# Optimization experiments

Hardware: AMD Instinct MI355X
Metric: run time of the kernel (lower is better)

## Reference

```python
import jax, jax.numpy as jnp
import numpy as np

HEADS = 16
DIM_HEAD = 64
SCALE = DIM_HEAD ** -0.5


def setup_inputs() -> dict:
    key = jax.random.key(0)
    ks = jax.random.split(key, 6)
    B, Nq, Nkv, D = 2, 512, 4096, 1024
    inner = HEADS * DIM_HEAD  # 1024
    s = 1.0 / np.sqrt(D)
    return {
        "q": jax.random.normal(ks[0], (B, Nq, D), jnp.float32),
        "kv": jax.random.normal(ks[1], (B, Nkv, D), jnp.float32),
        "mask": jnp.ones((B, Nkv), dtype=bool),
        "Wq": jax.random.normal(ks[2], (D, inner), jnp.float32) * s,
        "Wkv": jax.random.normal(ks[3], (D, 2 * inner), jnp.float32) * s,
        "Wo": jax.random.normal(ks[4], (inner, D), jnp.float32) * (1.0 / np.sqrt(inner)),
        "bo": jnp.zeros((D,), jnp.float32),
    }


def reference(q, kv, mask, Wq, Wkv, Wo, bo):
    B, Nq, D = q.shape
    Nkv = kv.shape[1]
    h, dh = HEADS, DIM_HEAD
    # projections
    qh = (q @ Wq).reshape(B, Nq, h, dh).transpose(0, 2, 1, 3)        # (B,h,Nq,dh)
    kvp = kv @ Wkv                                                    # (B,Nkv,2*inner)
    k, v = jnp.split(kvp, 2, axis=-1)
    kh = k.reshape(B, Nkv, h, dh).transpose(0, 2, 1, 3)              # (B,h,Nkv,dh)
    vh = v.reshape(B, Nkv, h, dh).transpose(0, 2, 1, 3)
    # scaled dot-product cross-attention
    attn = jnp.einsum("bhqd,bhkd->bhqk", qh, kh) * SCALE             # (B,h,Nq,Nkv)
    neg_inf = jnp.finfo(attn.dtype).min
    attn = jnp.where(mask[:, None, None, :], attn, neg_inf)
    attn = jax.nn.softmax(attn, axis=-1)
    out = jnp.einsum("bhqk,bhkd->bhqd", attn, vh)                    # (B,h,Nq,dh)
    out = out.transpose(0, 2, 1, 3).reshape(B, Nq, h * dh)
    return out @ Wo + bo
```

## Files before the change

### kernel.cpp

```cpp
#include <hip/hip_runtime.h>
#include <string.h>
#include <math.h>

typedef unsigned short u16;
typedef __bf16 bf16x8 __attribute__((ext_vector_type(8)));
typedef float floatx4 __attribute__((ext_vector_type(4)));

#define HEADS  16
#define DH     64
#define BATCH  2
#define NQ     512
#define NKV    4096
#define DMODEL 1024
#define INNER  1024
#define SCALE  0.125f
#define LOG2E  1.4426950408889634f
#define FM     12.0f
#define SPLIT  4
#define KEYS_PER_PART (NKV / SPLIT)
#define CH (KEYS_PER_PART / 64)

__device__ __forceinline__ u16 f2bf(float f) {
  union { __bf16 h; u16 u; } v; v.h = (__bf16)f; return v.u;
}

__device__ __forceinline__ void gll16(const u16* g, u16* l) {
  __builtin_amdgcn_global_load_lds(
      (const __attribute__((address_space(1))) unsigned int*)g,
      (__attribute__((address_space(3))) unsigned int*)l, 16, 0, 0);
}

__global__ __launch_bounds__(256) void prep(const float* __restrict__ q,
                                            const float* __restrict__ kv,
                                            const float* __restrict__ Wq,
                                            const float* __restrict__ Wkv,
                                            const float* __restrict__ Wo,
                                            u16* __restrict__ qb,
                                            u16* __restrict__ kvb,
                                            u16* __restrict__ Wqt,
                                            u16* __restrict__ Wkvt,
                                            u16* __restrict__ Wot) {
  __shared__ float tile[32][33];
  const int bx = blockIdx.x, tid = threadIdx.x;
  if (bx < 4608) {
    const float* x; u16* y; size_t i;
    if (bx < 512) { x = q;  y = qb;  i = (size_t)bx * 256 + tid; }
    else          { x = kv; y = kvb; i = (size_t)(bx - 512) * 256 + tid; }
    const float4* p = (const float4*)x + i * 2;
    float4 a = p[0], b = p[1];
    union { u16 s[8]; uint4 v; } o;
    o.s[0] = f2bf(a.x); o.s[1] = f2bf(a.y); o.s[2] = f2bf(a.z); o.s[3] = f2bf(a.w);
    o.s[4] = f2bf(b.x); o.s[5] = f2bf(b.y); o.s[6] = f2bf(b.z); o.s[7] = f2bf(b.w);
    *(uint4*)(y + i * 8) = o.v;
    return;
  }
  const float* W; u16* Wt; int K, N, n0, k0, t;
  if (bx < 5632)      { t = bx - 4608; W = Wq;  Wt = Wqt;  K = 1024; N = 1024; n0 = (t & 31) * 32; k0 = (t >> 5) * 32; }
  else if (bx < 7680) { t = bx - 5632; W = Wkv; Wt = Wkvt; K = 1024; N = 2048; n0 = (t & 63) * 32; k0 = (t >> 6) * 32; }
  else                { t = bx - 7680; W = Wo;  Wt = Wot;  K = 1024; N = 1024; n0 = (t & 31) * 32; k0 = (t >> 5) * 32; }
  const int tx = tid & 31, ty = tid >> 5;
  for (int i = 0; i < 32; i += 8)
    tile[ty + i][tx] = W[(size_t)(k0 + ty + i) * N + n0 + tx];
  __syncthreads();
  for (int i = 0; i < 32; i += 8)
    Wt[(size_t)(n0 + ty + i) * K + k0 + tx] = f2bf(tile[tx][ty + i]);
}

__global__ __launch_bounds__(256) void gemm_kv(const u16* __restrict__ A,
                                               const u16* __restrict__ Bt,
                                               u16* __restrict__ Kb,
                                               u16* __restrict__ vT) {
  const int K = DMODEL;
  __shared__ __align__(16) u16 As[128 * 64];
  __shared__ __align__(16) u16 Bs[128 * 64];
  const int tid  = threadIdx.x;
  const int lane = tid & 63, wave = tid >> 6;
  const int wr = wave >> 1, wc = wave & 1;
  const int l16 = lane & 15, quad = lane >> 4;
  const int bm = blockIdx.y, bn = blockIdx.x;
  const int r8 = lane >> 3;
  const int kb8 = (lane & 7) ^ r8;
  const u16* aP = A  + ((size_t)bm * 128 + wave * 8 + r8) * K + kb8 * 8;
  const u16* bP = Bt + ((size_t)bn * 128 + wave * 8 + r8) * K + kb8 * 8;

  floatx4 acc[4][4] = {};
  for (int k0 = 0; k0 < K; k0 += 64) {
#pragma unroll
    for (int p = 0; p < 4; ++p) {
      gll16(aP + (size_t)p * 32 * K + k0, As + p * 2048 + wave * 512);
      gll16(bP + (size_t)p * 32 * K + k0, Bs + p * 2048 + wave * 512);
    }
    __syncthreads();
    bf16x8 af[4][2], bfr[4][2];
#pragma unroll
    for (int i = 0; i < 4; ++i)
#pragma unroll
      for (int h2 = 0; h2 < 2; ++h2)
        af[i][h2] = *(const bf16x8*)&As[(wr * 64 + i * 16 + l16) * 64 +
                                        (((h2 * 4 + quad) ^ (l16 & 7)) << 3)];
#pragma unroll
    for (int j = 0; j < 4; ++j)
#pragma unroll
      for (int h2 = 0; h2 < 2; ++h2)
        bfr[j][h2] = *(const bf16x8*)&Bs[(wc * 64 + j * 16 + l16) * 64 +
                                         (((h2 * 4 + quad) ^ (l16 & 7)) << 3)];
#pragma unroll
    for (int i = 0; i < 4; ++i)
#pragma unroll
      for (int j = 0; j < 4; ++j) {
        acc[i][j] = __builtin_amdgcn_mfma_f32_16x16x32_bf16(af[i][0], bfr[j][0], acc[i][j], 0, 0, 0);
        acc[i][j] = __builtin_amdgcn_mfma_f32_16x16x32_bf16(af[i][1], bfr[j][1], acc[i][j], 0, 0, 0);
      }
    __syncthreads();
  }
  if (bn < 8) {
#pragma unroll
    for (int i = 0; i < 4; ++i) {
      const int rowb = bm * 128 + wr * 64 + i * 16 + quad * 4;
#pragma unroll
      for (int j = 0; j < 4; ++j) {
        const int col = bn * 128 + wc * 64 + j * 16 + l16;
#pragma unroll
        for (int r = 0; r < 4; ++r)
          Kb[(size_t)(rowb + r) * 1024 + col] = f2bf(acc[i][j][r]);
      }
    }
  } else {
    const int b = bm >> 5;
    const int tokb = (bm & 31) * 128;
#pragma unroll
    for (int i = 0; i < 4; ++i) {
      const int tok0 = tokb + wr * 64 + i * 16 + quad * 4;
#pragma unroll
      for (int j = 0; j < 4; ++j) {
        const int d = (bn - 8) * 128 + wc * 64 + j * 16 + l16;
        union { u16 s[4]; uint2 v; } pk;
#pragma unroll
        for (int r = 0; r < 4; ++r) pk.s[r] = f2bf(acc[i][j][r]);
        *(uint2*)(vT + ((size_t)(b * 1024 + d)) * NKV + tok0) = pk.v;
      }
    }
  }
}

template<bool OUT_BF16>
__global__ __launch_bounds__(256) void gemm64(const u16* __restrict__ A,
                                              const u16* __restrict__ Bt,
                                              float* __restrict__ Cf,
                                              u16* __restrict__ Cb,
                                              const float* __restrict__ bias,
                                              int M, int N, int K) {
  __shared__ __align__(16) u16 As[64 * 64];
  __shared__ __align__(16) u16 Bs[64 * 64];
  const int tid = threadIdx.x;
  const int lane = tid & 63, wave = tid >> 6;
  const int wr = wave >> 1, wc = wave & 1;
  const int l16 = lane & 15, quad = lane >> 4;
  const int bm = blockIdx.y, bn = blockIdx.x;
  const int r0 = tid >> 3;
  const int kbs = (tid & 7) ^ (r0 & 7);
  const u16* aP0 = A  + ((size_t)bm * 64 + r0)      * K + kbs * 8;
  const u16* aP1 = A  + ((size_t)bm * 64 + r0 + 32) * K + kbs * 8;
  const u16* bP0 = Bt + ((size_t)bn * 64 + r0)      * K + kbs * 8;
  const u16* bP1 = Bt + ((size_t)bn * 64 + r0 + 32) * K + kbs * 8;
  u16* ldsA0 = As + wave * 512;
  u16* ldsA1 = As + 2048 + wave * 512;
  u16* ldsB0 = Bs + wave * 512;
  u16* ldsB1 = Bs + 2048 + wave * 512;

  floatx4 acc[2][2] = {};
  for (int k0 = 0; k0 < K; k0 += 64) {
    gll16(aP0 + k0, ldsA0);
    gll16(aP1 + k0, ldsA1);
    gll16(bP0 + k0, ldsB0);
    gll16(bP1 + k0, ldsB1);
    __syncthreads();
    bf16x8 af[2][2], bfr[2][2];
#pragma unroll
    for (int i = 0; i < 2; ++i)
#pragma unroll
      for (int kk = 0; kk < 2; ++kk)
        af[i][kk] = *(const bf16x8*)&As[(wr * 32 + i * 16 + l16) * 64 +
                                        (((kk * 4 + quad) ^ (l16 & 7)) << 3)];
#pragma unroll
    for (int j = 0; j < 2; ++j)
#pragma unroll
      for (int kk = 0; kk < 2; ++kk)
        bfr[j][kk] = *(const bf16x8*)&Bs[(wc * 32 + j * 16 + l16) * 64 +
                                         (((kk * 4 + quad) ^ (l16 & 7)) << 3)];
#pragma unroll
    for (int i = 0; i < 2; ++i)
#pragma unroll
      for (int j = 0; j < 2; ++j) {
        acc[i][j] = __builtin_amdgcn_mfma_f32_16x16x32_bf16(af[i][0], bfr[j][0], acc[i][j], 0, 0, 0);
        acc[i][j] = __builtin_amdgcn_mfma_f32_16x16x32_bf16(af[i][1], bfr[j][1], acc[i][j], 0, 0, 0);
      }
    __syncthreads();
  }
#pragma unroll
  for (int i = 0; i < 2; ++i) {
    const int rowb = bm * 64 + wr * 32 + i * 16 + quad * 4;
#pragma unroll
    for (int j = 0; j < 2; ++j) {
      const int col = bn * 64 + wc * 32 + j * 16 + l16;
#pragma unroll
      for (int r = 0; r < 4; ++r) {
        const size_t idx = (size_t)(rowb + r) * N + col;
        if (OUT_BF16) Cb[idx] = f2bf(acc[i][j][r]);
        else          Cf[idx] = acc[i][j][r] + bias[col];
      }
    }
  }
}

__global__ __launch_bounds__(256) void attn_part(const u16* __restrict__ Qh,
                                                 const u16* __restrict__ Kb,
                                                 const u16* __restrict__ vT,
                                                 const int* __restrict__ mask,
                                                 float* __restrict__ Opart,
                                                 float* __restrict__ Mst,
                                                 float* __restrict__ Lst) {
  __shared__ __align__(16) u16 Ks[64 * 64];
  __shared__ __align__(16) u16 Vs[2][64 * 64];
  __shared__ __align__(16) u16 QP[4608];
  __shared__ float Msk[64];
  const int tid = threadIdx.x;
  const int lane = tid & 63, w = tid >> 6;
  const int l16 = lane & 15, quad = lane >> 4;
  const int part = blockIdx.x & (SPLIT - 1);
  const int qt = (blockIdx.x >> 2) & 7;
  const int h  = (blockIdx.x >> 5) & 15;
  const int b  = blockIdx.x >> 9;
  const int rs = tid >> 2, d0 = (tid & 3) * 16;
  u16* Ps = QP + w * 1152;

  const int r8 = lane >> 3;
  const int kb8 = (lane & 7) ^ (r8 & 7);
  const int key00 = part * KEYS_PER_PART;
  const u16* kSrc = Kb + ((size_t)(b * NKV + key00 + w * 8 + r8)) * 1024 + h * DH + kb8 * 8;
  const u16* vSrc = vT + ((size_t)((b * 16 + h) * 64 + w * 8 + r8)) * NKV + key00 + kb8 * 8;
  u16* ldsK0 = Ks + w * 512;
  u16* ldsK1 = Ks + 2048 + w * 512;
  const int koA = (quad ^ (l16 & 7)) << 3;
  const int koB = ((quad + 4) ^ (l16 & 7)) << 3;

  bf16x8 bones;
  {
    union { u16 s[8]; bf16x8 v; } t1;
    const u16 o1 = (l16 == 0) ? (u16)0x3F80 : (u16)0;
#pragma unroll
    for (int i = 0; i < 8; ++i) t1.s[i] = o1;
    bones = t1.v;
  }

  {
    const uint4* p = (const uint4*)(Qh + ((size_t)(b * NQ + qt * 64 + rs)) * INNER + h * DH + d0);
    *(uint4*)&QP[rs * 72 + d0]     = p[0];
    *(uint4*)&QP[rs * 72 + d0 + 8] = p[1];
  }
  gll16(kSrc, ldsK0);
  gll16(kSrc + 32768, ldsK1);
  gll16(vSrc, Vs[0] + w * 512);
  gll16(vSrc + (size_t)32 * NKV, Vs[0] + 2048 + w * 512);
  float mk0 = 0.f;
  if (tid < 64) mk0 = (mask[(size_t)b * NKV + key00 + tid] != 0) ? -FM : -1e30f;
  __syncthreads();
  bf16x8 aq0 = *(const bf16x8*)&QP[(w * 16 + l16) * 72 + quad * 8];
  bf16x8 aq1 = *(const bf16x8*)&QP[(w * 16 + l16) * 72 + 32 + quad * 8];
  if (tid < 64) Msk[tid] = mk0;
  __syncthreads();

  floatx4 o[4] = {};
  floatx4 lacc = {0.f, 0.f, 0.f, 0.f};
  const float SC = SCALE * LOG2E;

  for (int c = 0; c < CH; ++c) {
    const u16* Vcur = Vs[c & 1];
#pragma unroll
    for (int nt = 0; nt < 4; ++nt) {
      bf16x8 b0 = *(const bf16x8*)&Ks[(nt * 16 + l16) * 64 + koA];
      bf16x8 b1 = *(const bf16x8*)&Ks[(nt * 16 + l16) * 64 + koB];
      floatx4 t = {0.f, 0.f, 0.f, 0.f};
      t = __builtin_amdgcn_mfma_f32_16x16x32_bf16(aq0, b0, t, 0, 0, 0);
      t = __builtin_amdgcn_mfma_f32_16x16x32_bf16(aq1, b1, t, 0, 0, 0);
      const float mk = Msk[nt * 16 + l16];
#pragma unroll
      for (int r = 0; r < 4; ++r)
        Ps[(quad * 4 + r) * 72 + nt * 16 + l16] = f2bf(exp2f(t[r] * SC + mk));
    }
    __syncthreads();
    if (c + 1 < CH) {
      gll16(kSrc + (size_t)(c + 1) * 65536, ldsK0);
      gll16(kSrc + (size_t)(c + 1) * 65536 + 32768, ldsK1);
      u16* vdst = Vs[(c + 1) & 1];
      gll16(vSrc + (c + 1) * 64, vdst + w * 512);
      gll16(vSrc + (c + 1) * 64 + (size_t)32 * NKV, vdst + 2048 + w * 512);
      if (tid < 64)
        Msk[tid] = (mask[(size_t)b * NKV + key00 + (c + 1) * 64 + tid] != 0) ? -FM : -1e30f;
    }
    bf16x8 ap0 = *(const bf16x8*)&Ps[l16 * 72 + quad * 8];
    bf16x8 ap1 = *(const bf16x8*)&Ps[l16 * 72 + 32 + quad * 8];
    lacc = __builtin_amdgcn_mfma_f32_16x16x32_bf16(ap0, bones, lacc, 0, 0, 0);
    lacc = __builtin_amdgcn_mfma_f32_16x16x32_bf16(ap1, bones, lacc, 0, 0, 0);
#pragma unroll
    for (int dt = 0; dt < 4; ++dt) {
      bf16x8 bv0 = *(const bf16x8*)&Vcur[(dt * 16 + l16) * 64 + koA];
      bf16x8 bv1 = *(const bf16x8*)&Vcur[(dt * 16 + l16) * 64 + koB];
      o[dt] = __builtin_amdgcn_mfma_f32_16x16x32_bf16(ap0, bv0, o[dt], 0, 0, 0);
      o[dt] = __builtin_amdgcn_mfma_f32_16x16x32_bf16(ap1, bv1, o[dt], 0, 0, 0);
    }
    __syncthreads();
  }
  const int pid = blockIdx.x;
#pragma unroll
  for (int r = 0; r < 4; ++r) {
    const int q = w * 16 + quad * 4 + r;
    if (l16 == 0) { Mst[pid * 64 + q] = FM; Lst[pid * 64 + q] = lacc[r]; }
#pragma unroll
    for (int dt = 0; dt < 4; ++dt)
      Opart[(size_t)pid * 4096 + q * 64 + dt * 16 + l16] = o[dt][r];
  }
}

__global__ __launch_bounds__(256) void attn_combine(const float* __restrict__ Opart,
                                                    const float* __restrict__ Mst,
                                                    const float* __restrict__ Lst,
                                                    u16* __restrict__ Out) {
  const int x = blockIdx.x;
  const int t = threadIdx.x;
  const int q = t >> 2, db = (t & 3) * 16;
  const int b = x >> 7, h = (x >> 3) & 15, qt = x & 7;
  float ms[SPLIT], ls[SPLIT];
#pragma unroll
  for (int s = 0; s < SPLIT; ++s) {
    ms[s] = Mst[(size_t)(x * SPLIT + s) * 64 + q];
    ls[s] = Lst[(size_t)(x * SPLIT + s) * 64 + q];
  }
  float M = fmaxf(fmaxf(ms[0], ms[1]), fmaxf(ms[2], ms[3]));
  float wgt[SPLIT], L = 0.f;
#pragma unroll
  for (int s = 0; s < SPLIT; ++s) { wgt[s] = exp2f(ms[s] - M); L += wgt[s] * ls[s]; }
  const float inv = 1.0f / L;
  float acc[16] = {};
#pragma unroll
  for (int s = 0; s < SPLIT; ++s) {
    const float4* p = (const float4*)&Opart[(size_t)(x * SPLIT + s) * 4096 + q * 64 + db];
    const float ws = wgt[s];
#pragma unroll
    for (int i = 0; i < 4; ++i) {
      float4 v = p[i];
      acc[i * 4 + 0] += ws * v.x; acc[i * 4 + 1] += ws * v.y;
      acc[i * 4 + 2] += ws * v.z; acc[i * 4 + 3] += ws * v.w;
    }
  }
  union { u16 s[16]; uint4 v[2]; } ou;
#pragma unroll
  for (int i = 0; i < 16; ++i) ou.s[i] = f2bf(acc[i] * inv);
  u16* dst = Out + ((size_t)(b * NQ + qt * 64 + q)) * INNER + h * DH + db;
  *(uint4*)dst = ou.v[0]; *(uint4*)(dst + 8) = ou.v[1];
}

extern "C" void kernel_launch(void* const* d_in, const int* in_sizes, int n_in,
                              void* d_out, int out_size, void* d_ws, size_t ws_size,
                              hipStream_t stream) {
  const float* q    = (const float*)d_in[0];
  const float* kv   = (const float*)d_in[1];
  const int*   mask = (const int*)d_in[2];
  const float* Wq   = (const float*)d_in[3];
  const float* Wkv  = (const float*)d_in[4];
  const float* Wo   = (const float*)d_in[5];
  const float* bo   = (const float*)d_in[6];
  float* out = (float*)d_out;

  char* ws = (char*)d_ws;
  u16*   qb    = (u16*)(ws);
  u16*   kvb   = (u16*)(ws + (2u << 20));
  float* Mst   = (float*)(ws);
  float* Lst   = (float*)(ws + (256u << 10));
  float* Opart = (float*)(ws + (2u << 20));
  u16* Wqt  = (u16*)(ws + (18u << 20));
  u16* Wkvt = (u16*)(ws + (20u << 20));
  u16* Wot  = (u16*)(ws + (24u << 20));
  u16* qh   = (u16*)(ws + (26u << 20));
  u16* Kb   = (u16*)(ws + (28u << 20));
  u16* vT   = (u16*)(ws + (44u << 20));
  u16* attn = (u16*)(ws + (60u << 20));

  prep<<<dim3(8704), 256, 0, stream>>>(q, kv, Wq, Wkv, Wo, qb, kvb, Wqt, Wkvt, Wot);
  gemm64<true><<<dim3(INNER / 64, (BATCH * NQ) / 64), 256, 0, stream>>>(
      qb, Wqt, nullptr, qh, nullptr, BATCH * NQ, INNER, DMODEL);
  gemm_kv<<<dim3(16, 64), 256, 0, stream>>>(kvb, Wkvt, Kb, vT);
  attn_part<<<dim3(BATCH * HEADS * (NQ / 64) * SPLIT), 256, 0, stream>>>(
      qh, Kb, vT, mask, Opart, Mst, Lst);
  attn_combine<<<dim3(BATCH * HEADS * (NQ / 64)), 256, 0, stream>>>(Opart, Mst, Lst, attn);
  gemm64<false><<<dim3(DMODEL / 64, (BATCH * NQ) / 64), 256, 0, stream>>>(
      attn, Wot, out, nullptr, bo, BATCH * NQ, DMODEL, INNER);
}
```

Baseline: 214.0 us.

## Rewrite KV GEMM with 256x128 tiles, triple-buffered async loads, and XCD-aware block remap

```diff
diff --git a/kernel.cpp b/kernel.cpp
--- a/kernel.cpp
+++ b/kernel.cpp
@@ -66,81 +66,112 @@
     Wt[(size_t)(n0 + ty + i) * K + k0 + tx] = f2bf(tile[tx][ty + i]);
 }
 
-__global__ __launch_bounds__(256) void gemm_kv(const u16* __restrict__ A,
-                                               const u16* __restrict__ Bt,
-                                               u16* __restrict__ Kb,
-                                               u16* __restrict__ vT) {
+#define KV_NT 16
+__global__ __launch_bounds__(512, 2) void gemm_kv(const u16* __restrict__ A,
+                                                  const u16* __restrict__ Bt,
+                                                  u16* __restrict__ Kb,
+                                                  u16* __restrict__ vT) {
   const int K = DMODEL;
-  __shared__ __align__(16) u16 As[128 * 64];
-  __shared__ __align__(16) u16 Bs[128 * 64];
+  __shared__ __align__(16) u16 As[3][256 * 64];
+  __shared__ __align__(16) u16 Bs[3][128 * 64];
   const int tid  = threadIdx.x;
   const int lane = tid & 63, wave = tid >> 6;
-  const int wr = wave >> 1, wc = wave & 1;
+  const int wr = wave >> 2, wc = wave & 3;
   const int l16 = lane & 15, quad = lane >> 4;
-  const int bm = blockIdx.y, bn = blockIdx.x;
+  const int d = blockIdx.x;
+  const int lg = (d & 7) * 64 + (d >> 3);
+  const int bm = lg >> 4, bn = lg & 15;
   const int r8 = lane >> 3;
   const int kb8 = (lane & 7) ^ r8;
-  const u16* aP = A  + ((size_t)bm * 128 + wave * 8 + r8) * K + kb8 * 8;
+  const u16* aP = A  + ((size_t)bm * 256 + wave * 8 + r8) * K + kb8 * 8;
   const u16* bP = Bt + ((size_t)bn * 128 + wave * 8 + r8) * K + kb8 * 8;
 
-  floatx4 acc[4][4] = {};
-  for (int k0 = 0; k0 < K; k0 += 64) {
-#pragma unroll
-    for (int p = 0; p < 4; ++p) {
-      gll16(aP + (size_t)p * 32 * K + k0, As + p * 2048 + wave * 512);
-      gll16(bP + (size_t)p * 32 * K + k0, Bs + p * 2048 + wave * 512);
-    }
-    __syncthreads();
-    bf16x8 af[4][2], bfr[4][2];
-#pragma unroll
-    for (int i = 0; i < 4; ++i)
+  floatx4 acc[8][2] = {};
+
+#define KV_STAGE(t_) { \
+    const int j_ = (t_) % 3; \
+    u16* aD = &As[j_][wave * 512]; \
+    u16* bD = &Bs[j_][wave * 512]; \
+    const size_t ko = (size_t)(t_) * 64; \
+    gll16(aP + ko,                       aD); \
+    gll16(aP +  64 * (size_t)K + ko,     aD +  64 * 64); \
+    gll16(aP + 128 * (size_t)K + ko,     aD + 128 * 64); \
+    gll16(aP + 192 * (size_t)K + ko,     aD + 192 * 64); \
+    gll16(bP + ko,                       bD); \
+    gll16(bP +  64 * (size_t)K + ko,     bD +  64 * 64); \
+  }
+
+  KV_STAGE(0);
+  KV_STAGE(1);
+
+  for (int t = 0; t < KV_NT; ++t) {
+    if (t + 2 < KV_NT) {
+      KV_STAGE(t + 2);
+      asm volatile("s_waitcnt vmcnt(12)" ::: "memory");
+    } else if (t + 1 < KV_NT) {
+      asm volatile("s_waitcnt vmcnt(6)" ::: "memory");
+    } else {
+      asm volatile("s_waitcnt vmcnt(0)" ::: "memory");
+    }
+    __builtin_amdgcn_s_barrier();
+    asm volatile("" ::: "memory");
+    const u16* Ab = As[t % 3];
+    const u16* Bb = Bs[t % 3];
+    bf16x8 af[8][2], bfr[2][2];
+#pragma unroll
+    for (int m = 0; m < 8; ++m)
 #pragma unroll
       for (int h2 = 0; h2 < 2; ++h2)
-        af[i][h2] = *(const bf16x8*)&As[(wr * 64 + i * 16 + l16) * 64 +
+        af[m][h2] = *(const bf16x8*)&Ab[(wr * 128 + m * 16 + l16) * 64 +
                                         (((h2 * 4 + quad) ^ (l16 & 7)) << 3)];
 #pragma unroll
-    for (int j = 0; j < 4; ++j)
+    for (int n = 0; n < 2; ++n)
 #pragma unroll
       for (int h2 = 0; h2 < 2; ++h2)
-        bfr[j][h2] = *(const bf16x8*)&Bs[(wc * 64 + j * 16 + l16) * 64 +
+        bfr[n][h2] = *(const bf16x8*)&Bb[(wc * 32 + n * 16 + l16) * 64 +
                                          (((h2 * 4 + quad) ^ (l16 & 7)) << 3)];
-#pragma unroll
-    for (int i = 0; i < 4; ++i)
-#pragma unroll
-      for (int j = 0; j < 4; ++j) {
-        acc[i][j] = __builtin_amdgcn_mfma_f32_16x16x32_bf16(af[i][0], bfr[j][0], acc[i][j], 0, 0, 0);
-        acc[i][j] = __builtin_amdgcn_mfma_f32_16x16x32_bf16(af[i][1], bfr[j][1], acc[i][j], 0, 0, 0);
+    __builtin_amdgcn_s_setprio(1);
+#pragma unroll
+    for (int m = 0; m < 8; ++m)
+#pragma unroll
+      for (int n = 0; n < 2; ++n) {
+        acc[m][n] = __builtin_amdgcn_mfma_f32_16x16x32_bf16(af[m][0], bfr[n][0], acc[m][n], 0, 0, 0);
+        acc[m][n] = __builtin_amdgcn_mfma_f32_16x16x32_bf16(af[m][1], bfr[n][1], acc[m][n], 0, 0, 0);
       }
-    __syncthreads();
-  }
+    __builtin_amdgcn_s_setprio(0);
+    asm volatile("" ::: "memory");
+    __builtin_amdgcn_s_barrier();
+  }
+
   if (bn < 8) {
 #pragma unroll
-    for (int i = 0; i < 4; ++i) {
-      const int rowb = bm * 128 + wr * 64 + i * 16 + quad * 4;
-#pragma unroll
-      for (int j = 0; j < 4; ++j) {
-        const int col = bn * 128 + wc * 64 + j * 16 + l16;
+    for (int m = 0; m < 8; ++m) {
+      const int rowb = bm * 256 + wr * 128 + m * 16 + quad * 4;
+#pragma unroll
+      for (int n = 0; n < 2; ++n) {
+        const int col = bn * 128 + wc * 32 + n * 16 + l16;
 #pragma unroll
         for (int r = 0; r < 4; ++r)
-          Kb[(size_t)(rowb + r) * 1024 + col] = f2bf(acc[i][j][r]);
+          Kb[(size_t)(rowb + r) * 1024 + col] = f2bf(acc[m][n][r]);
       }
     }
   } else {
-    const int b = bm >> 5;
-    const int tokb = (bm & 31) * 128;
-#pragma unroll
-    for (int i = 0; i < 4; ++i) {
-      const int tok0 = tokb + wr * 64 + i * 16 + quad * 4;
-#pragma unroll
-      for (int j = 0; j < 4; ++j) {
-        const int d = (bn - 8) * 128 + wc * 64 + j * 16 + l16;
+    const int b = bm >> 4;
+    const int tokb = (bm & 15) * 256;
+#pragma unroll
+    for (int m = 0; m < 8; ++m) {
+      const int tok0 = tokb + wr * 128 + m * 16 + quad * 4;
+#pragma unroll
+      for (int n = 0; n < 2; ++n) {
+        const int dd = (bn - 8) * 128 + wc * 32 + n * 16 + l16;
         union { u16 s[4]; uint2 v; } pk;
 #pragma unroll
-        for (int r = 0; r < 4; ++r) pk.s[r] = f2bf(acc[i][j][r]);
-        *(uint2*)(vT + ((size_t)(b * 1024 + d)) * NKV + tok0) = pk.v;
+        for (int r = 0; r < 4; ++r) pk.s[r] = f2bf(acc[m][n][r]);
+        *(uint2*)(vT + ((size_t)(b * 1024 + dd)) * NKV + tok0) = pk.v;
       }
     }
   }
+#undef KV_STAGE
 }
 
 template<bool OUT_BF16>
@@ -227,10 +258,12 @@
   const int tid = threadIdx.x;
   const int lane = tid & 63, w = tid >> 6;
   const int l16 = lane & 15, quad = lane >> 4;
-  const int part = blockIdx.x & (SPLIT - 1);
-  const int qt = (blockIdx.x >> 2) & 7;
-  const int h  = (blockIdx.x >> 5) & 15;
-  const int b  = blockIdx.x >> 9;
+  const int d_ = blockIdx.x;
+  const int lg = (d_ & 7) * 128 + (d_ >> 3);
+  const int qt   = lg & 7;
+  const int part = (lg >> 3) & 3;
+  const int h    = (lg >> 5) & 15;
+  const int b    = lg >> 9;
   const int rs = tid >> 2, d0 = (tid & 3) * 16;
   u16* Ps = QP + w * 1152;
 
@@ -311,7 +344,7 @@
     }
     __syncthreads();
   }
-  const int pid = blockIdx.x;
+  const int pid = (((b * 16 + h) * 8 + qt) * 4) + part;
 #pragma unroll
   for (int r = 0; r < 4; ++r) {
     const int q = w * 16 + quad * 4 + r;
@@ -389,7 +422,7 @@
   prep<<<dim3(8704), 256, 0, stream>>>(q, kv, Wq, Wkv, Wo, qb, kvb, Wqt, Wkvt, Wot);
   gemm64<true><<<dim3(INNER / 64, (BATCH * NQ) / 64), 256, 0, stream>>>(
       qb, Wqt, nullptr, qh, nullptr, BATCH * NQ, INNER, DMODEL);
-  gemm_kv<<<dim3(16, 64), 256, 0, stream>>>(kvb, Wkvt, Kb, vT);
+  gemm_kv<<<dim3(512), 512, 0, stream>>>(kvb, Wkvt, Kb, vT);
   attn_part<<<dim3(BATCH * HEADS * (NQ / 64) * SPLIT), 256, 0, stream>>>(
       qh, Kb, vT, mask, Opart, Mst, Lst);
   attn_combine<<<dim3(BATCH * HEADS * (NQ / 64)), 256, 0, stream>>>(Opart, Mst, Lst, attn);
```

New measurement: 217.0 us. About the same (+1.4%).

## Double-buffer GEMM LDS tiles and remap block order for XCD locality

Applied to the files above, without the earlier changes.

```diff
diff --git a/kernel.cpp b/kernel.cpp
--- a/kernel.cpp
+++ b/kernel.cpp
@@ -66,44 +66,60 @@
     Wt[(size_t)(n0 + ty + i) * K + k0 + tx] = f2bf(tile[tx][ty + i]);
 }
 
+#define KV_NT 16
 __global__ __launch_bounds__(256) void gemm_kv(const u16* __restrict__ A,
                                                const u16* __restrict__ Bt,
                                                u16* __restrict__ Kb,
                                                u16* __restrict__ vT) {
   const int K = DMODEL;
-  __shared__ __align__(16) u16 As[128 * 64];
-  __shared__ __align__(16) u16 Bs[128 * 64];
+  __shared__ __align__(16) u16 As[2][128 * 64];
+  __shared__ __align__(16) u16 Bs[2][128 * 64];
   const int tid  = threadIdx.x;
   const int lane = tid & 63, wave = tid >> 6;
   const int wr = wave >> 1, wc = wave & 1;
   const int l16 = lane & 15, quad = lane >> 4;
-  const int bm = blockIdx.y, bn = blockIdx.x;
+  const int d = blockIdx.x;
+  const int lg = (d & 7) * 128 + (d >> 3);
+  const int bm = lg >> 4, bn = lg & 15;
   const int r8 = lane >> 3;
   const int kb8 = (lane & 7) ^ r8;
   const u16* aP = A  + ((size_t)bm * 128 + wave * 8 + r8) * K + kb8 * 8;
   const u16* bP = Bt + ((size_t)bn * 128 + wave * 8 + r8) * K + kb8 * 8;
 
   floatx4 acc[4][4] = {};
-  for (int k0 = 0; k0 < K; k0 += 64) {
-#pragma unroll
-    for (int p = 0; p < 4; ++p) {
-      gll16(aP + (size_t)p * 32 * K + k0, As + p * 2048 + wave * 512);
-      gll16(bP + (size_t)p * 32 * K + k0, Bs + p * 2048 + wave * 512);
-    }
-    __syncthreads();
+
+#define KV_STAGE(t_) { \
+    const int j_ = (t_) & 1; \
+    const size_t ko = (size_t)(t_) * 64; \
+    _Pragma("unroll") \
+    for (int p = 0; p < 4; ++p) { \
+      gll16(aP + (size_t)p * 32 * K + ko, &As[j_][p * 2048 + wave * 512]); \
+      gll16(bP + (size_t)p * 32 * K + ko, &Bs[j_][p * 2048 + wave * 512]); \
+    } \
+  }
+
+  KV_STAGE(0);
+  asm volatile("s_waitcnt vmcnt(0)" ::: "memory");
+  __builtin_amdgcn_s_barrier();
+
+  for (int t = 0; t < KV_NT; ++t) {
+    if (t + 1 < KV_NT) KV_STAGE(t + 1);
+    const u16* Ab = As[t & 1];
+    const u16* Bb = Bs[t & 1];
     bf16x8 af[4][2], bfr[4][2];
 #pragma unroll
     for (int i = 0; i < 4; ++i)
 #pragma unroll
       for (int h2 = 0; h2 < 2; ++h2)
-        af[i][h2] = *(const bf16x8*)&As[(wr * 64 + i * 16 + l16) * 64 +
+        af[i][h2] = *(const bf16x8*)&Ab[(wr * 64 + i * 16 + l16) * 64 +
                                         (((h2 * 4 + quad) ^ (l16 & 7)) << 3)];
 #pragma unroll
     for (int j = 0; j < 4; ++j)
 #pragma unroll
       for (int h2 = 0; h2 < 2; ++h2)
-        bfr[j][h2] = *(const bf16x8*)&Bs[(wc * 64 + j * 16 + l16) * 64 +
+        bfr[j][h2] = *(const bf16x8*)&Bb[(wc * 64 + j * 16 + l16) * 64 +
                                          (((h2 * 4 + quad) ^ (l16 & 7)) << 3)];
+    __builtin_amdgcn_s_setprio(1);
 #pragma unroll
     for (int i = 0; i < 4; ++i)
 #pragma unroll
@@ -111,8 +127,11 @@
         acc[i][j] = __builtin_amdgcn_mfma_f32_16x16x32_bf16(af[i][0], bfr[j][0], acc[i][j], 0, 0, 0);
         acc[i][j] = __builtin_amdgcn_mfma_f32_16x16x32_bf16(af[i][1], bfr[j][1], acc[i][j], 0, 0, 0);
       }
-    __syncthreads();
-  }
+    __builtin_amdgcn_s_setprio(0);
+    asm volatile("s_waitcnt vmcnt(0)" ::: "memory");
+    __builtin_amdgcn_s_barrier();
+  }
+
   if (bn < 8) {
 #pragma unroll
     for (int i = 0; i < 4; ++i) {
@@ -133,14 +152,15 @@
       const int tok0 = tokb + wr * 64 + i * 16 + quad * 4;
 #pragma unroll
       for (int j = 0; j < 4; ++j) {
-        const int d = (bn - 8) * 128 + wc * 64 + j * 16 + l16;
+        const int dd = (bn - 8) * 128 + wc * 64 + j * 16 + l16;
         union { u16 s[4]; uint2 v; } pk;
 #pragma unroll
         for (int r = 0; r < 4; ++r) pk.s[r] = f2bf(acc[i][j][r]);
-        *(uint2*)(vT + ((size_t)(b * 1024 + d)) * NKV + tok0) = pk.v;
+        *(uint2*)(vT + ((size_t)(b * 1024 + dd)) * NKV + tok0) = pk.v;
       }
     }
   }
+#undef KV_STAGE
 }
 
 template<bool OUT_BF16>
@@ -150,8 +170,8 @@
                                               u16* __restrict__ Cb,
                                               const float* __restrict__ bias,
                                               int M, int N, int K) {
-  __shared__ __align__(16) u16 As[64 * 64];
-  __shared__ __align__(16) u16 Bs[64 * 64];
+  __shared__ __align__(16) u16 As[2][64 * 64];
+  __shared__ __align__(16) u16 Bs[2][64 * 64];
   const int tid = threadIdx.x;
   const int lane = tid & 63, wave = tid >> 6;
   const int wr = wave >> 1, wc = wave & 1;
@@ -163,31 +183,41 @@
   const u16* aP1 = A  + ((size_t)bm * 64 + r0 + 32) * K + kbs * 8;
   const u16* bP0 = Bt + ((size_t)bn * 64 + r0)      * K + kbs * 8;
   const u16* bP1 = Bt + ((size_t)bn * 64 + r0 + 32) * K + kbs * 8;
-  u16* ldsA0 = As + wave * 512;
-  u16* ldsA1 = As + 2048 + wave * 512;
-  u16* ldsB0 = Bs + wave * 512;
-  u16* ldsB1 = Bs + 2048 + wave * 512;
 
   floatx4 acc[2][2] = {};
-  for (int k0 = 0; k0 < K; k0 += 64) {
-    gll16(aP0 + k0, ldsA0);
-    gll16(aP1 + k0, ldsA1);
-    gll16(bP0 + k0, ldsB0);
-    gll16(bP1 + k0, ldsB1);
-    __syncthreads();
+  const int nt = K >> 6;
+
+#define G64_STAGE(t_) { \
+    const int j_ = (t_) & 1; \
+    const size_t ko = (size_t)(t_) * 64; \
+    gll16(aP0 + ko, &As[j_][wave * 512]); \
+    gll16(aP1 + ko, &As[j_][2048 + wave * 512]); \
+    gll16(bP0 + ko, &Bs[j_][wave * 512]); \
+    gll16(bP1 + ko, &Bs[j_][2048 + wave * 512]); \
+  }
+
+  G64_STAGE(0);
+  asm volatile("s_waitcnt vmcnt(0)" ::: "memory");
+  __builtin_amdgcn_s_barrier();
+
+  for (int t = 0; t < nt; ++t) {
+    if (t + 1 < nt) G64_STAGE(t + 1);
+    const u16* Ab = As[t & 1];
+    const u16* Bb = Bs[t & 1];
     bf16x8 af[2][2], bfr[2][2];
 #pragma unroll
     for (int i = 0; i < 2; ++i)
 #pragma unroll
       for (int kk = 0; kk < 2; ++kk)
-        af[i][kk] = *(const bf16x8*)&As[(wr * 32 + i * 16 + l16) * 64 +
+        af[i][kk] = *(const bf16x8*)&Ab[(wr * 32 + i * 16 + l16) * 64 +
                                         (((kk * 4 + quad) ^ (l16 & 7)) << 3)];
 #pragma unroll
     for (int j = 0; j < 2; ++j)
 #pragma unroll
       for (int kk = 0; kk < 2; ++kk)
-        bfr[j][kk] = *(const bf16x8*)&Bs[(wc * 32 + j * 16 + l16) * 64 +
-                                         (((kk * 4 + quad) ^ (l16 & 7)) << 3)];
+        bfr[j][kk] = *(const bf16x8*)&Bs[t & 1][(wc * 32 + j * 16 + l16) * 64 +
+                                               (((kk * 4 + quad) ^ (l16 & 7)) << 3)];
+    __builtin_amdgcn_s_setprio(1);
 #pragma unroll
     for (int i = 0; i < 2; ++i)
 #pragma unroll
@@ -195,8 +225,12 @@
         acc[i][j] = __builtin_amdgcn_mfma_f32_16x16x32_bf16(af[i][0], bfr[j][0], acc[i][j], 0, 0, 0);
         acc[i][j] = __builtin_amdgcn_mfma_f32_16x16x32_bf16(af[i][1], bfr[j][1], acc[i][j], 0, 0, 0);
       }
-    __syncthreads();
-  }
+    __builtin_amdgcn_s_setprio(0);
+    asm volatile("s_waitcnt vmcnt(0)" ::: "memory");
+    __builtin_amdgcn_s_barrier();
+    (void)Bb;
+  }
+#undef G64_STAGE
 #pragma unroll
   for (int i = 0; i < 2; ++i) {
     const int rowb = bm * 64 + wr * 32 + i * 16 + quad * 4;
@@ -227,10 +261,12 @@
   const int tid = threadIdx.x;
   const int lane = tid & 63, w = tid >> 6;
   const int l16 = lane & 15, quad = lane >> 4;
-  const int part = blockIdx.x & (SPLIT - 1);
-  const int qt = (blockIdx.x >> 2) & 7;
-  const int h  = (blockIdx.x >> 5) & 15;
-  const int b  = blockIdx.x >> 9;
+  const int d_ = blockIdx.x;
+  const int lg = (d_ & 7) * 128 + (d_ >> 3);
+  const int qt   = lg & 7;
+  const int part = (lg >> 3) & 3;
+  const int h    = (lg >> 5) & 15;
+  const int b    = lg >> 9;
   const int rs = tid >> 2, d0 = (tid & 3) * 16;
   u16* Ps = QP + w * 1152;
 
@@ -311,7 +347,7 @@
     }
     __syncthreads();
   }
-  const int pid = blockIdx.x;
+  const int pid = (((b * 16 + h) * 8 + qt) * 4) + part;
 #pragma unroll
   for (int r = 0; r < 4; ++r) {
     const int q = w * 16 + quad * 4 + r;
@@ -389,7 +425,7 @@
   prep<<<dim3(8704), 256, 0, stream>>>(q, kv, Wq, Wkv, Wo, qb, kvb, Wqt, Wkvt, Wot);
   gemm64<true><<<dim3(INNER / 64, (BATCH * NQ) / 64), 256, 0, stream>>>(
       qb, Wqt, nullptr, qh, nullptr, BATCH * NQ, INNER, DMODEL);
-  gemm_kv<<<dim3(16, 64), 256, 0, stream>>>(kvb, Wkvt, Kb, vT);
+  gemm_kv<<<dim3(1024), 256, 0, stream>>>(kvb, Wkvt, Kb, vT);
   attn_part<<<dim3(BATCH * HEADS * (NQ / 64) * SPLIT), 256, 0, stream>>>(
       qh, Kb, vT, mask, Opart, Mst, Lst);
   attn_combine<<<dim3(BATCH * HEADS * (NQ / 64)), 256, 0, stream>>>(Opart, Mst, Lst, attn);
```

Result: no change. 215.6 us (+0.7%).
